# Kernel tuning notes

Measured on AMD Instinct MI355X. Metric: run time of the kernel, lower is better.

## Reference

```python
import jax, jax.numpy as jnp
import numpy as np

B, P, S, FX, FY, D, DFF = 8, 1, 2048, 16, 16, 512, 2048


def _ln(x, g, b, eps=1e-6):
    m = jnp.mean(x, axis=-1, keepdims=True)
    v = jnp.var(x, axis=-1, keepdims=True)
    return g * (x - m) / jnp.sqrt(v + eps) + b


def setup_inputs() -> dict:
    key = jax.random.key(0)
    ks = jax.random.split(key, 16)
    sc = 0.02
    inp = {
        'inputs': jax.random.normal(ks[0], (B, P, S, FX), dtype=jnp.float32),
        'targets': jax.random.normal(ks[1], (B, P, S, FY), dtype=jnp.float32),
        # input projection Dense(d_model)
        'Wp': jax.random.normal(ks[2], (FX, D), dtype=jnp.float32) * sc,
        'bp': jnp.zeros((D,), jnp.float32),
        # attention projections wq/wk/wv/dense (all Dense(d_model))
        'Wq': jax.random.normal(ks[3], (D, D), dtype=jnp.float32) * sc,
        'bq': jnp.zeros((D,), jnp.float32),
        'Wk': jax.random.normal(ks[4], (D, D), dtype=jnp.float32) * sc,
        'bk': jnp.zeros((D,), jnp.float32),
        'Wv': jax.random.normal(ks[5], (D, D), dtype=jnp.float32) * sc,
        'bv': jnp.zeros((D,), jnp.float32),
        'Wo': jax.random.normal(ks[6], (D, D), dtype=jnp.float32) * sc,
        'bo': jnp.zeros((D,), jnp.float32),
        # layernorm 1 / 2
        'g1': jnp.ones((D,), jnp.float32),
        'beta1': jnp.zeros((D,), jnp.float32),
        'g2': jnp.ones((D,), jnp.float32),
        'beta2': jnp.zeros((D,), jnp.float32),
        # pointwise FFN Dense(dff, relu) -> Dense(d_model)
        'Wf1': jax.random.normal(ks[7], (D, DFF), dtype=jnp.float32) * sc,
        'bf1': jnp.zeros((DFF,), jnp.float32),
        'Wf2': jax.random.normal(ks[8], (DFF, D), dtype=jnp.float32) * sc,
        'bf2': jnp.zeros((D,), jnp.float32),
        # final output layer Dense(output_size)
        'Wfin': jax.random.normal(ks[9], (D, FY), dtype=jnp.float32) * sc,
        'bfin': jnp.zeros((FY,), jnp.float32),
    }
    return inp


def reference(inputs, targets, Wp, bp, Wq, bq, Wk, bk, Wv, bv, Wo, bo,
              g1, beta1, g2, beta2, Wf1, bf1, Wf2, bf2, Wfin, bfin):
    d = jnp.float32(Wp.shape[1])
    # projection_layer_ts then *sqrt(d_model)
    x = (inputs @ Wp + bp) * jnp.sqrt(d)                      # (B,P,S,D)
    q = x @ Wq + bq
    k = x @ Wk + bk
    v = x @ Wv + bv
    # with noise=False and no resampling, the per-step SMC recurrence equals
    # causal self-attention (at step t, K/V hold rows <= t, rest are zero-masked)
    logits = jnp.einsum('bpqd,bpkd->bpqk', q, k) / jnp.sqrt(d)  # (B,P,S,S)
    Sdim = x.shape[2]
    causal = jnp.tril(jnp.ones((Sdim, Sdim), dtype=bool))
    logits = jnp.where(causal, logits, jnp.float32(-1e9))
    attn = jax.nn.softmax(logits, axis=-1)                    # attention weights per step
    z = jnp.einsum('bpqk,bpkd->bpqd', attn, v)
    z = z @ Wo + bo
    # full_model: LN(z+x) -> FFN -> LN(ffn+out)
    out = _ln(z + x, g1, beta1)
    ff = jax.nn.relu(out @ Wf1 + bf1) @ Wf2 + bf2
    r = _ln(ff + out, g2, beta2)                              # R trajectory (B,P,S,D)
    pred = r @ Wfin + bfin                                    # (B,P,S,F_y)
    # no resampling (noise=False): R_resampl == R, pred_resampl == pred
    return (pred, pred, k, v, r, attn)
```

## Files before the change

kernel.cpp:

```cpp
#include <hip/hip_runtime.h>
#include <hip/hip_bf16.h>
#include <stdint.h>

#define BB 8
#define SS 2048
#define TT (BB*SS)
#define DD 512
#define DFFX 2048

static __device__ const float SQRTD  = 22.627416997969522f;
static __device__ const float INVSQD = 0.04419417382415922f;

typedef __attribute__((ext_vector_type(4))) float  f32x4_t;
typedef __attribute__((ext_vector_type(8))) __bf16 bf16x8_t;
typedef __attribute__((ext_vector_type(4))) __bf16 bf16x4_t;
typedef __attribute__((ext_vector_type(2))) __bf16 bf16x2_t;

static __device__ __forceinline__ bf16x8_t mk_frag(bf16x4_t lo, bf16x4_t hi) {
  return __builtin_shufflevector(lo, hi, 0, 1, 2, 3, 4, 5, 6, 7);
}

typedef __attribute__((address_space(1))) const unsigned int g_u32;
typedef __attribute__((address_space(3))) unsigned int lds_u32;
static __device__ __forceinline__ void gld16(const void* g, void* l) {
  __builtin_amdgcn_global_load_lds((g_u32*)g, (lds_u32*)l, 16, 0, 0);
}

__global__ __launch_bounds__(256) void transpose_conv_f32(
    const float* __restrict__ src, __bf16* __restrict__ dst, int R, int C) {
  __shared__ float tile[32][33];
  int c0 = blockIdx.x * 32, r0 = blockIdx.y * 32;
  int tx = threadIdx.x & 31, ty = threadIdx.x >> 5;
#pragma unroll
  for (int i = 0; i < 4; i++)
    tile[ty + 8*i][tx] = src[(size_t)(r0 + ty + 8*i) * C + c0 + tx];
  __syncthreads();
#pragma unroll
  for (int i = 0; i < 4; i++)
    dst[(size_t)(c0 + ty + 8*i) * R + r0 + tx] = (__bf16)tile[tx][ty + 8*i];
}

__global__ __launch_bounds__(256) void fold_kernel(
    const float* __restrict__ Wp, const float* __restrict__ bp,
    const float* __restrict__ Wq, const float* __restrict__ bq,
    const float* __restrict__ Wk, const float* __restrict__ bk,
    const float* __restrict__ Wv, const float* __restrict__ bv,
    float* __restrict__ Wfold, float* __restrict__ bfold) {
  __shared__ float wp[16][512];
  __shared__ float bps[512];
  for (int i = threadIdx.x; i < 16 * 512; i += 256) wp[i >> 9][i & 511] = Wp[i];
  for (int i = threadIdx.x; i < 512; i += 256) bps[i] = bp[i];
  __syncthreads();
  const int cl = threadIdx.x & 15, r = threadIdx.x >> 4;
  const int cg = blockIdx.x * 16 + cl;
  const int sub = cg >> 9, wc = cg & 511;
  const float* W = sub == 0 ? Wq : sub == 1 ? Wk : Wv;
  const float* bb = sub == 0 ? bq : sub == 1 ? bk : bv;
  float acc = 0.f, bacc = 0.f;
  for (int k = 0; k < 512; k += 4) {
    const float4 wpv = *(const float4*)&wp[r][k];
    const float g0 = W[(size_t)k * 512 + wc];
    const float g1 = W[(size_t)(k + 1) * 512 + wc];
    const float g2 = W[(size_t)(k + 2) * 512 + wc];
    const float g3 = W[(size_t)(k + 3) * 512 + wc];
    acc += wpv.x * g0 + wpv.y * g1 + wpv.z * g2 + wpv.w * g3;
    if (r == 0) {
      const float4 b4 = *(const float4*)&bps[k];
      bacc += b4.x * g0 + b4.y * g1 + b4.z * g2 + b4.w * g3;
    }
  }
  Wfold[(size_t)r * 1536 + cg] = acc * SQRTD;
  if (r == 0) bfold[cg] = bacc * SQRTD + bb[wc];
}

__global__ __launch_bounds__(256) void smallk_kernel(
    const float* __restrict__ inp,
    const float* __restrict__ Wfold, const float* __restrict__ bfold,
    const float* __restrict__ Wp, const float* __restrict__ bp,
    __bf16* __restrict__ qb, __bf16* __restrict__ kb, __bf16* __restrict__ vb,
    __bf16* __restrict__ xb, float* __restrict__ o_k, float* __restrict__ o_v) {
  const int sl = blockIdx.y;
  const float* W; const float* bias; int ldw; float scale;
  __bf16* ob; float* fo;
  if (sl == 3) { W = Wp; bias = bp; ldw = 512; scale = SQRTD; ob = xb; fo = nullptr; }
  else {
    W = Wfold + sl * 512; bias = bfold + sl * 512; ldw = 1536; scale = 1.f;
    ob = sl == 0 ? qb : sl == 1 ? kb : vb;
    fo = sl == 0 ? (float*)nullptr : sl == 1 ? o_k : o_v;
  }
  __shared__ float ivl[16][16];
  const int tid = threadIdx.x;
  ivl[tid >> 4][tid & 15] = inp[(size_t)blockIdx.x * 256 + tid];
  const int c0 = 2 * tid;
  float w0[16], w1[16];
#pragma unroll
  for (int r = 0; r < 16; r++) {
    w0[r] = W[(size_t)r * ldw + c0];
    w1[r] = W[(size_t)r * ldw + c0 + 1];
  }
  const float bb0 = bias[c0], bb1 = bias[c0 + 1];
  __syncthreads();
#pragma unroll 4
  for (int tt = 0; tt < 16; ++tt) {
    const float4 i0 = *(const float4*)&ivl[tt][0];
    const float4 i1 = *(const float4*)&ivl[tt][4];
    const float4 i2 = *(const float4*)&ivl[tt][8];
    const float4 i3 = *(const float4*)&ivl[tt][12];
    float a0, a1;
    a0  = i0.x * w0[0];   a1  = i0.x * w1[0];
    a0 += i0.y * w0[1];   a1 += i0.y * w1[1];
    a0 += i0.z * w0[2];   a1 += i0.z * w1[2];
    a0 += i0.w * w0[3];   a1 += i0.w * w1[3];
    a0 += i1.x * w0[4];   a1 += i1.x * w1[4];
    a0 += i1.y * w0[5];   a1 += i1.y * w1[5];
    a0 += i1.z * w0[6];   a1 += i1.z * w1[6];
    a0 += i1.w * w0[7];   a1 += i1.w * w1[7];
    a0 += i2.x * w0[8];   a1 += i2.x * w1[8];
    a0 += i2.y * w0[9];   a1 += i2.y * w1[9];
    a0 += i2.z * w0[10];  a1 += i2.z * w1[10];
    a0 += i2.w * w0[11];  a1 += i2.w * w1[11];
    a0 += i3.x * w0[12];  a1 += i3.x * w1[12];
    a0 += i3.y * w0[13];  a1 += i3.y * w1[13];
    a0 += i3.z * w0[14];  a1 += i3.z * w1[14];
    a0 += i3.w * w0[15];  a1 += i3.w * w1[15];
    const float v0 = (a0 + bb0) * scale;
    const float v1 = (a1 + bb1) * scale;
    const size_t t = (size_t)blockIdx.x * 16 + tt;
    bf16x2_t pv; pv[0] = (__bf16)v0; pv[1] = (__bf16)v1;
    *(bf16x2_t*)(ob + t * 512 + c0) = pv;
    if (fo) {
      float2 fv; fv.x = v0; fv.y = v1;
      *(float2*)(fo + t * 512 + c0) = fv;
    }
  }
}

template <bool CTRI, bool CAUSAL, bool RELU, bool RES, bool SCALE, bool CT>
__global__ __launch_bounds__(256) void gemm128(
    const __bf16* __restrict__ A, const __bf16* __restrict__ Bt,
    const float* __restrict__ bias, const __bf16* __restrict__ Res,
    __bf16* __restrict__ Cb, float* __restrict__ Cf,
    int N, int K, size_t aBatch, size_t bBatch, size_t cBatch) {
  const int n0 = blockIdx.x * 128, m0 = blockIdx.y * 128;
  if (CTRI && n0 > m0 + 127) return;
  __shared__ __align__(16) __bf16 As[3 * 128 * 32];
  __shared__ __align__(16) __bf16 Bs[3 * 128 * 32];
  const int tid = threadIdx.x, lane = tid & 63, wave = tid >> 6;
  const int l15 = lane & 15, g = lane >> 4;
  const int wr = wave >> 1, wc = wave & 1;

  const int srow0 = wave * 32 + (lane >> 2);
  const int srow1 = srow0 + 16;
  const int sc0 = (((lane & 3) ^ ((srow0 >> 1) & 3)) << 4);
  const int sc1 = (((lane & 3) ^ ((srow1 >> 1) & 3)) << 4);
  const size_t aOff = (size_t)blockIdx.z * aBatch;
  const size_t bOff = (size_t)blockIdx.z * bBatch;
  const size_t cOff = (size_t)blockIdx.z * cBatch;
  const char* ga0 = (const char*)(A + aOff + (size_t)(m0 + srow0) * K) + sc0;
  const char* ga1 = (const char*)(A + aOff + (size_t)(m0 + srow1) * K) + sc1;
  const char* gb0 = (const char*)(Bt + bOff + (size_t)(n0 + srow0) * K) + sc0;
  const char* gb1 = (const char*)(Bt + bOff + (size_t)(n0 + srow1) * K) + sc1;

  const int plo = (g >> 1) ^ ((l15 >> 1) & 3);
  const int aof0 = (wr * 64 + l15) * 64 + plo * 16 + (g & 1) * 8;
  const int bof0 = (wc * 64 + l15) * 64 + plo * 16 + (g & 1) * 8;

  f32x4_t acc[4][4];
#pragma unroll
  for (int i = 0; i < 4; i++)
#pragma unroll
    for (int j = 0; j < 4; j++) acc[i][j] = (f32x4_t){0.f, 0.f, 0.f, 0.f};

  auto STAGE = [&](const int buf, const int k0) {
    const size_t kb = (size_t)k0 * 2;
    char* la = (char*)As + buf * 8192 + wave * 2048;
    char* lb = (char*)Bs + buf * 8192 + wave * 2048;
    gld16(ga0 + kb, la);
    gld16(ga1 + kb, la + 1024);
    gld16(gb0 + kb, lb);
    gld16(gb1 + kb, lb + 1024);
  };
  auto COMPUTE = [&](const int buf) {
    const char* AsB = (const char*)As + buf * 8192;
    const char* BsB = (const char*)Bs + buf * 8192;
    bf16x8_t af[4], bfr[4];
#pragma unroll
    for (int i = 0; i < 4; i++) {
      const int ao = aof0 + i * 1024;
      af[i] = mk_frag(*(const bf16x4_t*)(AsB + ao),
                      *(const bf16x4_t*)(AsB + (ao ^ 32)));
      const int bo = bof0 + i * 1024;
      bfr[i] = mk_frag(*(const bf16x4_t*)(BsB + bo),
                       *(const bf16x4_t*)(BsB + (bo ^ 32)));
    }
#pragma unroll
    for (int i = 0; i < 4; i++)
#pragma unroll
      for (int j = 0; j < 4; j++)
        acc[i][j] = __builtin_amdgcn_mfma_f32_16x16x32_bf16(af[i], bfr[j], acc[i][j], 0, 0, 0);
  };

  const int kend = CAUSAL ? (m0 + 128) : K;
  const int nt = kend >> 5;
  STAGE(0, 0);
  STAGE(1, 32);
  STAGE(2, 64);
  int cur = 0;
  for (int t = 0; t < nt; ++t) {
    const int rem = nt - 1 - t;
    if (rem >= 2)      asm volatile("s_waitcnt vmcnt(8)" ::: "memory");
    else if (rem == 1) asm volatile("s_waitcnt vmcnt(4)" ::: "memory");
    else               asm volatile("s_waitcnt vmcnt(0)" ::: "memory");
    __builtin_amdgcn_s_barrier();
    COMPUTE(cur);
    __builtin_amdgcn_s_barrier();
    if (t + 3 < nt) STAGE(cur, (t + 3) << 5);
    cur = (cur == 2) ? 0 : cur + 1;
  }

#pragma unroll
  for (int i = 0; i < 4; i++) {
#pragma unroll
    for (int j = 0; j < 4; j++) {
      const int col = n0 + wc * 64 + j * 16 + l15;
      if (CT) {
        const int row0 = m0 + wr * 64 + i * 16 + g * 4;
        bf16x4_t tv;
#pragma unroll
        for (int r = 0; r < 4; r++) tv[r] = (__bf16)acc[i][j][r];
        *(bf16x4_t*)(Cb + cOff + (size_t)col * SS + row0) = tv;
      } else {
        const float bv = bias ? bias[col] : 0.f;
#pragma unroll
        for (int r = 0; r < 4; r++) {
          const int row = m0 + wr * 64 + i * 16 + g * 4 + r;
          float v = acc[i][j][r];
          if (SCALE) v *= INVSQD;
          v += bv;
          if (RELU) v = fmaxf(v, 0.f);
          if (RES) v += (float)Res[cOff + (size_t)row * N + col];
          const size_t cidx = cOff + (size_t)row * N + col;
          if (Cb) Cb[cidx] = (__bf16)v;
          if (Cf) Cf[cidx] = v;
        }
      }
    }
  }
}

__global__ __launch_bounds__(256) void softmax_kernel(
    float* __restrict__ att, __bf16* __restrict__ pb) {
  const int t = blockIdx.x * 4 + (threadIdx.x >> 6);
  const int gq = t & (SS - 1);
  const int lane = threadIdx.x & 63;
  float* row = att + (size_t)t * SS;
  __bf16* prow = pb + (size_t)t * SS;
  const int nch = (gq >> 9) + 1;
  float x[32];
  float m = -1e30f;
#pragma unroll
  for (int ch = 0; ch < 4; ch++) {
    float* xp = &x[ch * 8];
    if (ch < nch) {
      const int c0 = ch * 512 + lane * 8;
      bf16x8_t v = *(const bf16x8_t*)(prow + c0);
#pragma unroll
      for (int j = 0; j < 8; j++) {
        const float f = (float)v[j];
        xp[j] = (c0 + j <= gq) ? f : -1e30f;
        m = fmaxf(m, xp[j]);
      }
    } else {
#pragma unroll
      for (int j = 0; j < 8; j++) xp[j] = -1e30f;
    }
  }
#pragma unroll
  for (int off = 1; off < 64; off <<= 1) m = fmaxf(m, __shfl_xor(m, off, 64));
  float s = 0.f;
#pragma unroll
  for (int i = 0; i < 32; i++) { x[i] = __expf(x[i] - m); s += x[i]; }
#pragma unroll
  for (int off = 1; off < 64; off <<= 1) s += __shfl_xor(s, off, 64);
  const float inv = 1.f / s;
#pragma unroll
  for (int ch = 0; ch < 4; ch++) {
    const int c0 = ch * 512 + lane * 8;
    float o[8];
    bf16x8_t ov;
#pragma unroll
    for (int j = 0; j < 8; j++) {
      const float pv = x[ch * 8 + j] * inv;
      o[j] = pv;
      ov[j] = (__bf16)pv;
    }
    float4 f0, f1;
    f0.x = o[0]; f0.y = o[1]; f0.z = o[2]; f0.w = o[3];
    f1.x = o[4]; f1.y = o[5]; f1.z = o[6]; f1.w = o[7];
    *(float4*)(row + c0) = f0;
    *(float4*)(row + c0 + 4) = f1;
    *(bf16x8_t*)(prow + c0) = ov;
  }
}

__global__ __launch_bounds__(256) void ln_kernel(
    const __bf16* __restrict__ X, const float* __restrict__ gam,
    const float* __restrict__ bet, __bf16* __restrict__ Ob, float* __restrict__ Of) {
  const int t = blockIdx.x * 4 + (threadIdx.x >> 6);
  const int lane = threadIdx.x & 63;
  const int d0 = lane * 8;
  bf16x8_t xv = *(const bf16x8_t*)(X + (size_t)t * DD + d0);
  float x[8];
#pragma unroll
  for (int j = 0; j < 8; j++) x[j] = (float)xv[j];
  float s = 0.f, sq = 0.f;
#pragma unroll
  for (int j = 0; j < 8; j++) { s += x[j]; sq += x[j] * x[j]; }
#pragma unroll
  for (int off = 1; off < 64; off <<= 1) {
    s += __shfl_xor(s, off, 64);
    sq += __shfl_xor(sq, off, 64);
  }
  const float mean = s * (1.f / 512.f);
  const float var = sq * (1.f / 512.f) - mean * mean;
  const float rstd = rsqrtf(var + 1e-6f);
  float4 g0 = *(const float4*)(gam + d0), g1v = *(const float4*)(gam + d0 + 4);
  float4 b0 = *(const float4*)(bet + d0), b1v = *(const float4*)(bet + d0 + 4);
  float gg[8] = {g0.x, g0.y, g0.z, g0.w, g1v.x, g1v.y, g1v.z, g1v.w};
  float bb2[8] = {b0.x, b0.y, b0.z, b0.w, b1v.x, b1v.y, b1v.z, b1v.w};
  float o[8];
#pragma unroll
  for (int j = 0; j < 8; j++) o[j] = (x[j] - mean) * rstd * gg[j] + bb2[j];
  if (Ob) {
    bf16x8_t ov;
#pragma unroll
    for (int j = 0; j < 8; j++) ov[j] = (__bf16)o[j];
    *(bf16x8_t*)(Ob + (size_t)t * DD + d0) = ov;
  }
  if (Of) {
    float4 f0; f0.x = o[0]; f0.y = o[1]; f0.z = o[2]; f0.w = o[3];
    float4 f1; f1.x = o[4]; f1.y = o[5]; f1.z = o[6]; f1.w = o[7];
    *(float4*)(Of + (size_t)t * DD + d0) = f0;
    *(float4*)(Of + (size_t)t * DD + d0 + 4) = f1;
  }
}

__global__ __launch_bounds__(256) void final_kernel(
    const float* __restrict__ Rm, const float* __restrict__ Wfin,
    const float* __restrict__ bfin, float* __restrict__ P1, float* __restrict__ P2) {
  __shared__ float wfs[512][17];
  for (int i = threadIdx.x; i < 512 * 16; i += 256) wfs[i >> 4][i & 15] = Wfin[i];
  __syncthreads();
  const int tl = threadIdx.x >> 4, n = threadIdx.x & 15;
  const int t = blockIdx.x * 16 + tl;
  const float* rp = Rm + (size_t)t * DD;
  float acc = 0.f;
#pragma unroll 4
  for (int k = 0; k < 512; k += 4) {
    float4 rv = *(const float4*)(rp + k);
    acc += rv.x * wfs[k][n] + rv.y * wfs[k + 1][n] + rv.z * wfs[k + 2][n] + rv.w * wfs[k + 3][n];
  }
  const float v = acc + bfin[n];
  P1[(size_t)t * 16 + n] = v;
  P2[(size_t)t * 16 + n] = v;
}

extern "C" void kernel_launch(void* const* d_in, const int* in_sizes, int n_in,
                              void* d_out, int out_size, void* d_ws, size_t ws_size,
                              hipStream_t stream) {
  const float* inp  = (const float*)d_in[0];
  const float* Wp   = (const float*)d_in[2];
  const float* bp   = (const float*)d_in[3];
  const float* Wq   = (const float*)d_in[4];
  const float* bq   = (const float*)d_in[5];
  const float* Wk   = (const float*)d_in[6];
  const float* bk   = (const float*)d_in[7];
  const float* Wv   = (const float*)d_in[8];
  const float* bv   = (const float*)d_in[9];
  const float* Wo   = (const float*)d_in[10];
  const float* bo   = (const float*)d_in[11];
  const float* g1   = (const float*)d_in[12];
  const float* be1  = (const float*)d_in[13];
  const float* g2   = (const float*)d_in[14];
  const float* be2  = (const float*)d_in[15];
  const float* Wf1  = (const float*)d_in[16];
  const float* bf1  = (const float*)d_in[17];
  const float* Wf2  = (const float*)d_in[18];
  const float* bf2  = (const float*)d_in[19];
  const float* Wfin = (const float*)d_in[20];
  const float* bfin = (const float*)d_in[21];
  (void)in_sizes; (void)n_in; (void)out_size; (void)ws_size;

  float* out = (float*)d_out;
  float* o_pred1 = out;
  float* o_pred2 = out + 262144;
  float* o_k     = out + 524288;
  float* o_v     = out + 8912896;
  float* o_r     = out + 17301504;
  float* o_att   = out + 25690112;

  char* base = (char*)d_ws;
  size_t off = 0;
  auto takeB = [&](size_t bytes) -> char* {
    char* p = base + off;
    off += (bytes + 255) & ~(size_t)255;
    return p;
  };
  float*  Wfold = (float*)takeB((size_t)16 * 1536 * 4);
  float*  bfold = (float*)takeB((size_t)1536 * 4);
  __bf16* Wo_t  = (__bf16*)takeB((size_t)DD * DD * 2);
  __bf16* Wf1_t = (__bf16*)takeB((size_t)DD * DFFX * 2);
  __bf16* Wf2_t = (__bf16*)takeB((size_t)DD * DFFX * 2);
  __bf16* xb    = (__bf16*)takeB((size_t)TT * DD * 2);
  __bf16* qbuf  = (__bf16*)takeB((size_t)TT * DD * 2);
  __bf16* kbuf  = (__bf16*)takeB((size_t)TT * DD * 2);
  __bf16* vbuf  = (__bf16*)takeB((size_t)TT * DD * 2);
  __bf16* vwt   = (__bf16*)takeB((size_t)TT * DD * 2);
  __bf16* h1b   = (__bf16*)takeB((size_t)TT * DD * 2);
  __bf16* lninb = (__bf16*)takeB((size_t)TT * DD * 2);
  __bf16* ffb   = (__bf16*)takeB((size_t)TT * DFFX * 2);
  __bf16* pb    = ffb;

  transpose_conv_f32<<<dim3(16, 16), 256, 0, stream>>>(Wo, Wo_t, DD, DD);
  transpose_conv_f32<<<dim3(64, 16), 256, 0, stream>>>(Wf1, Wf1_t, DD, DFFX);
  transpose_conv_f32<<<dim3(16, 64), 256, 0, stream>>>(Wf2, Wf2_t, DFFX, DD);

  fold_kernel<<<dim3(96), 256, 0, stream>>>(Wp, bp, Wq, bq, Wk, bk, Wv, bv,
                                            Wfold, bfold);

  smallk_kernel<<<dim3(TT / 16, 4), 256, 0, stream>>>(
      inp, Wfold, bfold, Wp, bp, qbuf, kbuf, vbuf, xb, o_k, o_v);

  gemm128<true, false, false, false, true, false><<<dim3(16, 16, BB), 256, 0, stream>>>(
      qbuf, kbuf, nullptr, nullptr, pb, nullptr, SS, DD,
      (size_t)SS * DD, (size_t)SS * DD, (size_t)SS * SS);

  gemm128<false, false, false, false, false, true><<<dim3(4, 16, BB), 256, 0, stream>>>(
      vbuf, Wo_t, nullptr, nullptr, vwt, nullptr, DD, DD,
      (size_t)SS * DD, 0, (size_t)SS * DD);

  softmax_kernel<<<dim3(TT / 4), 256, 0, stream>>>(o_att, pb);

  gemm128<false, true, false, true, false, false><<<dim3(4, 16, BB), 256, 0, stream>>>(
      pb, vwt, bo, xb, lninb, nullptr, DD, SS,
      (size_t)SS * SS, (size_t)DD * SS, (size_t)SS * DD);

  ln_kernel<<<dim3(TT / 4), 256, 0, stream>>>(lninb, g1, be1, h1b, nullptr);

  gemm128<false, false, true, false, false, false><<<dim3(16, 128, 1), 256, 0, stream>>>(
      h1b, Wf1_t, bf1, nullptr, ffb, nullptr, DFFX, DD, 0, 0, 0);
  gemm128<false, false, false, true, false, false><<<dim3(4, 128, 1), 256, 0, stream>>>(
      ffb, Wf2_t, bf2, h1b, lninb, nullptr, DD, DFFX, 0, 0, 0);

  ln_kernel<<<dim3(TT / 4), 256, 0, stream>>>(lninb, g2, be2, nullptr, o_r);
  final_kernel<<<dim3(TT / 16), 256, 0, stream>>>(o_r, Wfin, bfin, o_pred1, o_pred2);
}
```

Before: 475.5 us.

## Pair causal PV row tiles per block, merge transposes, trim softmax bf16 writes

```diff
diff --git a/kernel.cpp b/kernel.cpp
--- a/kernel.cpp
+++ b/kernel.cpp
@@ -26,11 +26,18 @@
   __builtin_amdgcn_global_load_lds((g_u32*)g, (lds_u32*)l, 16, 0, 0);
 }
 
-__global__ __launch_bounds__(256) void transpose_conv_f32(
-    const float* __restrict__ src, __bf16* __restrict__ dst, int R, int C) {
+__global__ __launch_bounds__(256) void transpose_conv3(
+    const float* __restrict__ Wo, const float* __restrict__ Wf1,
+    const float* __restrict__ Wf2, __bf16* __restrict__ Wo_t,
+    __bf16* __restrict__ Wf1_t, __bf16* __restrict__ Wf2_t) {
+  const int bx = blockIdx.x;
+  const float* src; __bf16* dst; int C, R, gx, gy;
+  if (bx < 256)       { src = Wo;  dst = Wo_t;  R = 512;  C = 512;  gx = bx & 15;  gy = bx >> 4; }
+  else if (bx < 1280) { const int b = bx - 256;  src = Wf1; dst = Wf1_t; R = 512;  C = 2048; gx = b & 63; gy = b >> 6; }
+  else                { const int b = bx - 1280; src = Wf2; dst = Wf2_t; R = 2048; C = 512;  gx = b & 15; gy = b >> 4; }
   __shared__ float tile[32][33];
-  int c0 = blockIdx.x * 32, r0 = blockIdx.y * 32;
-  int tx = threadIdx.x & 31, ty = threadIdx.x >> 5;
+  const int c0 = gx * 32, r0 = gy * 32;
+  const int tx = threadIdx.x & 31, ty = threadIdx.x >> 5;
 #pragma unroll
   for (int i = 0; i < 4; i++)
     tile[ty + 8*i][tx] = src[(size_t)(r0 + ty + 8*i) * C + c0 + tx];
@@ -135,14 +142,14 @@
   }
 }
 
-template <bool CTRI, bool CAUSAL, bool RELU, bool RES, bool SCALE, bool CT>
+template <bool CTRI, bool CAUSAL, bool RELU, bool RES, bool SCALE, bool CT, bool PAIR>
 __global__ __launch_bounds__(256) void gemm128(
     const __bf16* __restrict__ A, const __bf16* __restrict__ Bt,
     const float* __restrict__ bias, const __bf16* __restrict__ Res,
     __bf16* __restrict__ Cb, float* __restrict__ Cf,
     int N, int K, size_t aBatch, size_t bBatch, size_t cBatch) {
-  const int n0 = blockIdx.x * 128, m0 = blockIdx.y * 128;
-  if (CTRI && n0 > m0 + 127) return;
+  const int n0 = blockIdx.x * 128;
+  if (CTRI && !PAIR && n0 > (int)blockIdx.y * 128 + 127) return;
   __shared__ __align__(16) __bf16 As[3 * 128 * 32];
   __shared__ __align__(16) __bf16 Bs[3 * 128 * 32];
   const int tid = threadIdx.x, lane = tid & 63, wave = tid >> 6;
@@ -156,8 +163,6 @@
   const size_t aOff = (size_t)blockIdx.z * aBatch;
   const size_t bOff = (size_t)blockIdx.z * bBatch;
   const size_t cOff = (size_t)blockIdx.z * cBatch;
-  const char* ga0 = (const char*)(A + aOff + (size_t)(m0 + srow0) * K) + sc0;
-  const char* ga1 = (const char*)(A + aOff + (size_t)(m0 + srow1) * K) + sc1;
   const char* gb0 = (const char*)(Bt + bOff + (size_t)(n0 + srow0) * K) + sc0;
   const char* gb1 = (const char*)(Bt + bOff + (size_t)(n0 + srow1) * K) + sc1;
 
@@ -165,83 +170,93 @@
   const int aof0 = (wr * 64 + l15) * 64 + plo * 16 + (g & 1) * 8;
   const int bof0 = (wc * 64 + l15) * 64 + plo * 16 + (g & 1) * 8;
 
-  f32x4_t acc[4][4];
-#pragma unroll
-  for (int i = 0; i < 4; i++)
-#pragma unroll
-    for (int j = 0; j < 4; j++) acc[i][j] = (f32x4_t){0.f, 0.f, 0.f, 0.f};
-
-  auto STAGE = [&](const int buf, const int k0) {
-    const size_t kb = (size_t)k0 * 2;
-    char* la = (char*)As + buf * 8192 + wave * 2048;
-    char* lb = (char*)Bs + buf * 8192 + wave * 2048;
-    gld16(ga0 + kb, la);
-    gld16(ga1 + kb, la + 1024);
-    gld16(gb0 + kb, lb);
-    gld16(gb1 + kb, lb + 1024);
-  };
-  auto COMPUTE = [&](const int buf) {
-    const char* AsB = (const char*)As + buf * 8192;
-    const char* BsB = (const char*)Bs + buf * 8192;
-    bf16x8_t af[4], bfr[4];
+  const int nhalf = PAIR ? 2 : 1;
+#pragma unroll
+  for (int half = 0; half < nhalf; ++half) {
+    const int mb = (half == 0) ? (int)blockIdx.y
+                               : (2 * (int)gridDim.y - 1 - (int)blockIdx.y);
+    const int m0 = mb * 128;
+    const char* ga0 = (const char*)(A + aOff + (size_t)(m0 + srow0) * K) + sc0;
+    const char* ga1 = (const char*)(A + aOff + (size_t)(m0 + srow1) * K) + sc1;
+
+    f32x4_t acc[4][4];
+#pragma unroll
+    for (int i = 0; i < 4; i++)
+#pragma unroll
+      for (int j = 0; j < 4; j++) acc[i][j] = (f32x4_t){0.f, 0.f, 0.f, 0.f};
+
+    auto STAGE = [&](const int buf, const int k0) {
+      const size_t kb = (size_t)k0 * 2;
+      char* la = (char*)As + buf * 8192 + wave * 2048;
+      char* lb = (char*)Bs + buf * 8192 + wave * 2048;
+      gld16(ga0 + kb, la);
+      gld16(ga1 + kb, la + 1024);
+      gld16(gb0 + kb, lb);
+      gld16(gb1 + kb, lb + 1024);
+    };
+    auto COMPUTE = [&](const int buf) {
+      const char* AsB = (const char*)As + buf * 8192;
+      const char* BsB = (const char*)Bs + buf * 8192;
+      bf16x8_t af[4], bfr[4];
+#pragma unroll
+      for (int i = 0; i < 4; i++) {
+        const int ao = aof0 + i * 1024;
+        af[i] = mk_frag(*(const bf16x4_t*)(AsB + ao),
+                        *(const bf16x4_t*)(AsB + (ao ^ 32)));
+        const int bo = bof0 + i * 1024;
+        bfr[i] = mk_frag(*(const bf16x4_t*)(BsB + bo),
+                         *(const bf16x4_t*)(BsB + (bo ^ 32)));
+      }
+#pragma unroll
+      for (int i = 0; i < 4; i++)
+#pragma unroll
+        for (int j = 0; j < 4; j++)
+          acc[i][j] = __builtin_amdgcn_mfma_f32_16x16x32_bf16(af[i], bfr[j], acc[i][j], 0, 0, 0);
+    };
+
+    const int kend = CAUSAL ? (m0 + 128) : K;
+    const int nt = kend >> 5;
+    STAGE(0, 0);
+    STAGE(1, 32);
+    STAGE(2, 64);
+    int cur = 0;
+    for (int t = 0; t < nt; ++t) {
+      const int rem = nt - 1 - t;
+      if (rem >= 2)      asm volatile("s_waitcnt vmcnt(8)" ::: "memory");
+      else if (rem == 1) asm volatile("s_waitcnt vmcnt(4)" ::: "memory");
+      else               asm volatile("s_waitcnt vmcnt(0)" ::: "memory");
+      __builtin_amdgcn_s_barrier();
+      COMPUTE(cur);
+      __builtin_amdgcn_s_barrier();
+      if (t + 3 < nt) STAGE(cur, (t + 3) << 5);
+      cur = (cur == 2) ? 0 : cur + 1;
+    }
+
 #pragma unroll
     for (int i = 0; i < 4; i++) {
-      const int ao = aof0 + i * 1024;
-      af[i] = mk_frag(*(const bf16x4_t*)(AsB + ao),
-                      *(const bf16x4_t*)(AsB + (ao ^ 32)));
-      const int bo = bof0 + i * 1024;
-      bfr[i] = mk_frag(*(const bf16x4_t*)(BsB + bo),
-                       *(const bf16x4_t*)(BsB + (bo ^ 32)));
-    }
-#pragma unroll
-    for (int i = 0; i < 4; i++)
-#pragma unroll
-      for (int j = 0; j < 4; j++)
-        acc[i][j] = __builtin_amdgcn_mfma_f32_16x16x32_bf16(af[i], bfr[j], acc[i][j], 0, 0, 0);
-  };
-
-  const int kend = CAUSAL ? (m0 + 128) : K;
-  const int nt = kend >> 5;
-  STAGE(0, 0);
-  STAGE(1, 32);
-  STAGE(2, 64);
-  int cur = 0;
-  for (int t = 0; t < nt; ++t) {
-    const int rem = nt - 1 - t;
-    if (rem >= 2)      asm volatile("s_waitcnt vmcnt(8)" ::: "memory");
-    else if (rem == 1) asm volatile("s_waitcnt vmcnt(4)" ::: "memory");
-    else               asm volatile("s_waitcnt vmcnt(0)" ::: "memory");
-    __builtin_amdgcn_s_barrier();
-    COMPUTE(cur);
-    __builtin_amdgcn_s_barrier();
-    if (t + 3 < nt) STAGE(cur, (t + 3) << 5);
-    cur = (cur == 2) ? 0 : cur + 1;
-  }
-
-#pragma unroll
-  for (int i = 0; i < 4; i++) {
-#pragma unroll
-    for (int j = 0; j < 4; j++) {
-      const int col = n0 + wc * 64 + j * 16 + l15;
-      if (CT) {
-        const int row0 = m0 + wr * 64 + i * 16 + g * 4;
-        bf16x4_t tv;
-#pragma unroll
-        for (int r = 0; r < 4; r++) tv[r] = (__bf16)acc[i][j][r];
-        *(bf16x4_t*)(Cb + cOff + (size_t)col * SS + row0) = tv;
-      } else {
-        const float bv = bias ? bias[col] : 0.f;
-#pragma unroll
-        for (int r = 0; r < 4; r++) {
-          const int row = m0 + wr * 64 + i * 16 + g * 4 + r;
-          float v = acc[i][j][r];
-          if (SCALE) v *= INVSQD;
-          v += bv;
-          if (RELU) v = fmaxf(v, 0.f);
-          if (RES) v += (float)Res[cOff + (size_t)row * N + col];
-          const size_t cidx = cOff + (size_t)row * N + col;
-          if (Cb) Cb[cidx] = (__bf16)v;
-          if (Cf) Cf[cidx] = v;
+#pragma unroll
+      for (int j = 0; j < 4; j++) {
+        const int col = n0 + wc * 64 + j * 16 + l15;
+        if (CT) {
+          const int row0 = m0 + wr * 64 + i * 16 + g * 4;
+          bf16x4_t tv;
+#pragma unroll
+          for (int r = 0; r < 4; r++) tv[r] = (__bf16)acc[i][j][r];
+          *(bf16x4_t*)(Cb + cOff + (size_t)col * SS + row0) = tv;
+        } else {
+          const float bv = bias ? bias[col] : 0.f;
+#pragma unroll
+          for (int r = 0; r < 4; r++) {
+            const int row = m0 + wr * 64 + i * 16 + g * 4 + r;
+            float v = acc[i][j][r];
+            if (SCALE) v *= INVSQD;
+            v += bv;
+            if (RELU) v = fmaxf(v, 0.f);
+            if (RES) v += (float)Res[cOff + (size_t)row * N + col];
+            const size_t cidx = cOff + (size_t)row * N + col;
+            if (Cb) Cb[cidx] = (__bf16)v;
+            if (Cf) Cf[cidx] = v;
+          }
         }
       }
     }
@@ -256,6 +271,7 @@
   float* row = att + (size_t)t * SS;
   __bf16* prow = pb + (size_t)t * SS;
   const int nch = (gq >> 9) + 1;
+  const int wlim = ((gq & ~127) + 128 + 511) >> 9;
   float x[32];
   float m = -1e30f;
 #pragma unroll
@@ -299,7 +315,7 @@
     f1.x = o[4]; f1.y = o[5]; f1.z = o[6]; f1.w = o[7];
     *(float4*)(row + c0) = f0;
     *(float4*)(row + c0 + 4) = f1;
-    *(bf16x8_t*)(prow + c0) = ov;
+    if (ch < wlim) *(bf16x8_t*)(prow + c0) = ov;
   }
 }
 
@@ -421,9 +437,7 @@
   __bf16* ffb   = (__bf16*)takeB((size_t)TT * DFFX * 2);
   __bf16* pb    = ffb;
 
-  transpose_conv_f32<<<dim3(16, 16), 256, 0, stream>>>(Wo, Wo_t, DD, DD);
-  transpose_conv_f32<<<dim3(64, 16), 256, 0, stream>>>(Wf1, Wf1_t, DD, DFFX);
-  transpose_conv_f32<<<dim3(16, 64), 256, 0, stream>>>(Wf2, Wf2_t, DFFX, DD);
+  transpose_conv3<<<dim3(2304), 256, 0, stream>>>(Wo, Wf1, Wf2, Wo_t, Wf1_t, Wf2_t);
 
   fold_kernel<<<dim3(96), 256, 0, stream>>>(Wp, bp, Wq, bq, Wk, bk, Wv, bv,
                                             Wfold, bfold);
@@ -431,25 +445,25 @@
   smallk_kernel<<<dim3(TT / 16, 4), 256, 0, stream>>>(
       inp, Wfold, bfold, Wp, bp, qbuf, kbuf, vbuf, xb, o_k, o_v);
 
-  gemm128<true, false, false, false, true, false><<<dim3(16, 16, BB), 256, 0, stream>>>(
+  gemm128<true, false, false, false, true, false, false><<<dim3(16, 16, BB), 256, 0, stream>>>(
       qbuf, kbuf, nullptr, nullptr, pb, nullptr, SS, DD,
       (size_t)SS * DD, (size_t)SS * DD, (size_t)SS * SS);
 
-  gemm128<false, false, false, false, false, true><<<dim3(4, 16, BB), 256, 0, stream>>>(
+  gemm128<false, false, false, false, false, true, false><<<dim3(4, 16, BB), 256, 0, stream>>>(
       vbuf, Wo_t, nullptr, nullptr, vwt, nullptr, DD, DD,
       (size_t)SS * DD, 0, (size_t)SS * DD);
 
   softmax_kernel<<<dim3(TT / 4), 256, 0, stream>>>(o_att, pb);
 
-  gemm128<false, true, false, true, false, false><<<dim3(4, 16, BB), 256, 0, stream>>>(
+  gemm128<false, true, false, true, false, false, true><<<dim3(4, 8, BB), 256, 0, stream>>>(
       pb, vwt, bo, xb, lninb, nullptr, DD, SS,
       (size_t)SS * SS, (size_t)DD * SS, (size_t)SS * DD);
 
   ln_kernel<<<dim3(TT / 4), 256, 0, stream>>>(lninb, g1, be1, h1b, nullptr);
 
-  gemm128<false, false, true, false, false, false><<<dim3(16, 128, 1), 256, 0, stream>>>(
+  gemm128<false, false, true, false, false, false, false><<<dim3(16, 128, 1), 256, 0, stream>>>(
       h1b, Wf1_t, bf1, nullptr, ffb, nullptr, DFFX, DD, 0, 0, 0);
-  gemm128<false, false, false, true, false, false><<<dim3(4, 128, 1), 256, 0, stream>>>(
+  gemm128<false, false, false, true, false, false, false><<<dim3(4, 128, 1), 256, 0, stream>>>(
       ffb, Wf2_t, bf2, h1b, lninb, nullptr, DD, DFFX, 0, 0, 0);
 
   ln_kernel<<<dim3(TT / 4), 256, 0, stream>>>(lninb, g2, be2, nullptr, o_r);
```

After: 472.2 us. About the same (-0.7%).
